# Kernel tuning notes

Hardware: AMD Instinct MI355X
Metric: run time of the kernel (lower is better)

## Reference

```python
import jax, jax.numpy as jnp
import numpy as np

B, S, D, H = 4, 2048, 768, 12
DK = D // H


def setup_inputs() -> dict:
    key = jax.random.key(0)
    ks = jax.random.split(key, 12)
    s = 1.0 / np.sqrt(D)
    return {
        "query": jax.random.normal(ks[0], (B, S, D), jnp.float32),
        "key_": jax.random.normal(ks[1], (B, S, D), jnp.float32),
        "value": jax.random.normal(ks[2], (B, S, D), jnp.float32),
        "mask": jax.random.randint(ks[3], (B, S), 0, 2, jnp.int32),
        # nn.Linear weights are (out_features, in_features); y = x @ W.T + b
        "Wq": jax.random.normal(ks[4], (D, D), jnp.float32) * s,
        "bq": jnp.zeros((D,), jnp.float32),
        "Wk": jax.random.normal(ks[5], (D, D), jnp.float32) * s,
        "bk": jnp.zeros((D,), jnp.float32),
        "Wv": jax.random.normal(ks[6], (D, D), jnp.float32) * s,
        "bv": jnp.zeros((D,), jnp.float32),
        "Wo": jax.random.normal(ks[7], (D, D), jnp.float32) * s,
        "bo": jnp.zeros((D,), jnp.float32),
    }


def reference(query, key_, value, mask, Wq, bq, Wk, bk, Wv, bv, Wo, bo):
    b = query.shape[0]
    # QKV projections, split heads: (B, S, D) -> (B, H, S, DK)
    def proj(x, W, bia):
        y = x @ W.T + bia
        return y.reshape(b, -1, H, DK).transpose(0, 2, 1, 3)

    q = proj(query, Wq, bq)
    k = proj(key_, Wk, bk)
    v = proj(value, Wv, bv)

    # Scaled dot-product attention with full [B, H, S, S] score matrix
    scores = jnp.einsum("bhqd,bhkd->bhqk", q, k) / jnp.sqrt(jnp.float32(DK))
    # mask: (B, S) broadcast over heads and query positions; masked_fill(mask==0, -1e9)
    scores = jnp.where(mask[:, None, None, :] == 0, jnp.float32(-1e9), scores)
    attn = jax.nn.softmax(scores, axis=-1)
    x = jnp.einsum("bhqk,bhkd->bhqd", attn, v)  # (B, H, S, DK)

    # merge heads and output projection
    x = x.transpose(0, 2, 1, 3).reshape(b, -1, H * DK)
    return x @ Wo.T + bo
```

## Files before the change

### kernel.cpp

```cpp
#include <hip/hip_runtime.h>
#include <math.h>

#define B_  4
#define S_  2048
#define D_  768
#define H_  12
#define DK_ 64
#define M_  (B_ * S_)
#define NBH_ (B_ * H_)

typedef float f32x4 __attribute__((ext_vector_type(4)));
typedef float f32x16 __attribute__((ext_vector_type(16)));
typedef __bf16 bf16x8 __attribute__((ext_vector_type(8)));
typedef unsigned u32x4v __attribute__((ext_vector_type(4)));

static __device__ __forceinline__ unsigned short f2bf(float f) {
    unsigned u = __builtin_bit_cast(unsigned, f);
    u += 0x7fffu + ((u >> 16) & 1u);
    return (unsigned short)(u >> 16);
}

static __device__ __forceinline__ unsigned cvt_pk_bf16(float lo, float hi) {
    unsigned r;
    asm("v_cvt_pk_bf16_f32 %0, %1, %2" : "=v"(r) : "v"(lo), "v"(hi));
    return r;
}

static __device__ __forceinline__ void proj_body(
    const float* __restrict__ X, const float* __restrict__ W,
    const float* __restrict__ bias, void* __restrict__ outp, const int mode,
    const float oscale)
{
    __shared__ __align__(16) unsigned short As[2][128 * 32];
    __shared__ __align__(16) unsigned short Bs[2][128 * 32];

    const int t  = threadIdx.x;
    const int l  = t & 63;
    const int w  = t >> 6;
    const int lr = l & 15;
    const int lg = l >> 4;
    const int wm = w >> 1;
    const int wn = w & 1;
    const int m0 = blockIdx.x * 128;
    const int n0 = blockIdx.y * 128;

    const int v0r = t >> 2,         v0s = t & 3;
    const int v1r = (t + 256) >> 2, v1s = (t + 256) & 3;
    const int off0 = v0r * 32 + ((v0s ^ ((v0r >> 1) & 3)) << 3);
    const int off1 = v1r * 32 + ((v1s ^ ((v1r >> 1) & 3)) << 3);
    const float* xg0 = X + (size_t)(m0 + v0r) * D_ + v0s * 8;
    const float* xg1 = X + (size_t)(m0 + v1r) * D_ + v1s * 8;
    const float* wg0 = W + (size_t)(n0 + v0r) * D_ + v0s * 8;
    const float* wg1 = W + (size_t)(n0 + v1r) * D_ + v1s * 8;

    float4 pxa, pxb, pxc, pxd, pwa, pwb, pwc, pwd;

#define PROJ_LOAD(K0) do { \
        pxa = *(const float4*)(xg0 + (K0)); pxb = *(const float4*)(xg0 + (K0) + 4); \
        pxc = *(const float4*)(xg1 + (K0)); pxd = *(const float4*)(xg1 + (K0) + 4); \
        pwa = *(const float4*)(wg0 + (K0)); pwb = *(const float4*)(wg0 + (K0) + 4); \
        pwc = *(const float4*)(wg1 + (K0)); pwd = *(const float4*)(wg1 + (K0) + 4); \
    } while (0)

#define PROJ_STORE(BUF) do { \
        u32x4v xa_, xb_, wa_, wb_; \
        xa_.x = cvt_pk_bf16(pxa.x, pxa.y); xa_.y = cvt_pk_bf16(pxa.z, pxa.w); \
        xa_.z = cvt_pk_bf16(pxb.x, pxb.y); xa_.w = cvt_pk_bf16(pxb.z, pxb.w); \
        xb_.x = cvt_pk_bf16(pxc.x, pxc.y); xb_.y = cvt_pk_bf16(pxc.z, pxc.w); \
        xb_.z = cvt_pk_bf16(pxd.x, pxd.y); xb_.w = cvt_pk_bf16(pxd.z, pxd.w); \
        wa_.x = cvt_pk_bf16(pwa.x, pwa.y); wa_.y = cvt_pk_bf16(pwa.z, pwa.w); \
        wa_.z = cvt_pk_bf16(pwb.x, pwb.y); wa_.w = cvt_pk_bf16(pwb.z, pwb.w); \
        wb_.x = cvt_pk_bf16(pwc.x, pwc.y); wb_.y = cvt_pk_bf16(pwc.z, pwc.w); \
        wb_.z = cvt_pk_bf16(pwd.x, pwd.y); wb_.w = cvt_pk_bf16(pwd.z, pwd.w); \
        *(u32x4v*)&As[BUF][off0] = xa_; \
        *(u32x4v*)&As[BUF][off1] = xb_; \
        *(u32x4v*)&Bs[BUF][off0] = wa_; \
        *(u32x4v*)&Bs[BUF][off1] = wb_; \
    } while (0)

    f32x4 acc[4][4];
#pragma unroll
    for (int mi = 0; mi < 4; mi++)
#pragma unroll
        for (int ni = 0; ni < 4; ni++) acc[mi][ni] = (f32x4){0.f, 0.f, 0.f, 0.f};

    const int fsw = (lr >> 1) & 3;

    PROJ_LOAD(0);
    PROJ_STORE(0);
    __syncthreads();

    for (int kt = 0; kt < 24; kt++) {
        const int cur = kt & 1;
        const bool more = (kt < 23);

        if (more) PROJ_LOAD((kt + 1) * 32);

        bf16x8 af[4], bfr[4];
#pragma unroll
        for (int mi = 0; mi < 4; mi++) {
            int row = wm * 64 + mi * 16 + lr;
            af[mi] = *(const bf16x8*)&As[cur][row * 32 + ((lg ^ fsw) << 3)];
        }
#pragma unroll
        for (int ni = 0; ni < 4; ni++) {
            int row = wn * 64 + ni * 16 + lr;
            bfr[ni] = *(const bf16x8*)&Bs[cur][row * 32 + ((lg ^ fsw) << 3)];
        }
#pragma unroll
        for (int mi = 0; mi < 4; mi++)
#pragma unroll
            for (int ni = 0; ni < 4; ni++)
                acc[mi][ni] = __builtin_amdgcn_mfma_f32_16x16x32_bf16(
                    af[mi], bfr[ni], acc[mi][ni], 0, 0, 0);

        if (more) PROJ_STORE(cur ^ 1);
        __syncthreads();
    }

#undef PROJ_LOAD
#undef PROJ_STORE

    const int mrow0 = m0 + wm * 64;
    const int ncol0 = n0 + wn * 64;
    if (mode == 1) {
        float* out = (float*)outp;
#pragma unroll
        for (int mi = 0; mi < 4; mi++)
#pragma unroll
            for (int ni = 0; ni < 4; ni++) {
                int n = ncol0 + ni * 16 + lr;
                float bv = bias[n];
#pragma unroll
                for (int j = 0; j < 4; j++) {
                    int m = mrow0 + mi * 16 + 4 * lg + j;
                    out[(size_t)m * D_ + n] = acc[mi][ni][j] + bv;
                }
            }
    } else if (mode == 0) {
        unsigned short* out = (unsigned short*)outp;
#pragma unroll
        for (int mi = 0; mi < 4; mi++)
#pragma unroll
            for (int ni = 0; ni < 4; ni++) {
                int n = ncol0 + ni * 16 + lr;
                int h = n >> 6, dk = n & 63;
                float bv = bias[n];
#pragma unroll
                for (int j = 0; j < 4; j++) {
                    int m = mrow0 + mi * 16 + 4 * lg + j;
                    int b = m >> 11, s = m & (S_ - 1);
                    out[((size_t)(b * H_ + h) * S_ + s) * DK_ + dk] =
                        f2bf((acc[mi][ni][j] + bv) * oscale);
                }
            }
    } else {
        unsigned short* out = (unsigned short*)outp;
#pragma unroll
        for (int mi = 0; mi < 4; mi++)
#pragma unroll
            for (int ni = 0; ni < 4; ni++) {
                int n = ncol0 + ni * 16 + lr;
                int h = n >> 6, dk = n & 63;
                float bv = bias[n];
                int m = mrow0 + mi * 16 + 4 * lg;
                int b = m >> 11, s = m & (S_ - 1);
                uint2 o;
                o.x = cvt_pk_bf16(acc[mi][ni][0] + bv, acc[mi][ni][1] + bv);
                o.y = cvt_pk_bf16(acc[mi][ni][2] + bv, acc[mi][ni][3] + bv);
                *(uint2*)&out[((size_t)(b * H_ + h) * DK_ + dk) * S_ + s] = o;
            }
    }
}

__global__ __launch_bounds__(256) void proj_qkv(
    const float* __restrict__ Xq, const float* __restrict__ Xk,
    const float* __restrict__ Xv,
    const float* __restrict__ Wq, const float* __restrict__ bq,
    const float* __restrict__ Wk, const float* __restrict__ bk,
    const float* __restrict__ Wv, const float* __restrict__ bv,
    unsigned short* __restrict__ Qb, unsigned short* __restrict__ Kb,
    unsigned short* __restrict__ VT)
{
    const int z = blockIdx.z;
    const float* X    = (z == 0) ? Xq : (z == 1) ? Xk : Xv;
    const float* W    = (z == 0) ? Wq : (z == 1) ? Wk : Wv;
    const float* bias = (z == 0) ? bq : (z == 1) ? bk : bv;
    void* out         = (z == 0) ? (void*)Qb : (z == 1) ? (void*)Kb : (void*)VT;
    const int mode    = (z == 2) ? 2 : 0;
    const float osc   = (z == 0) ? 0.125f : 1.0f;
    proj_body(X, W, bias, out, mode, osc);
}

__global__ __launch_bounds__(256) void proj_mfma(
    const float* __restrict__ X, const float* __restrict__ W,
    const float* __restrict__ bias, void* __restrict__ outp, const int mode,
    const float oscale)
{
    proj_body(X, W, bias, outp, mode, oscale);
}

__global__ __launch_bounds__(256) void attn_mfma(
    const unsigned short* __restrict__ Qb, const unsigned short* __restrict__ Kb,
    const unsigned short* __restrict__ VTb, const int* __restrict__ mask,
    float* __restrict__ O)
{
    __shared__ __align__(16) unsigned short Ks[2][64 * 64];
    __shared__ __align__(16) unsigned short Vs[2][64 * 64];

    const int tid = threadIdx.x;
    const int w  = tid >> 6;
    const int l  = tid & 63;
    const int q  = l & 31;
    const int hl = l >> 5;

    const int bh = blockIdx.x % NBH_;
    const int qt = blockIdx.x / NBH_;
    const int b  = bh / H_;
    const int hh = bh - b * H_;
    const int q0 = qt * 128 + w * 32;

    const unsigned short* qp = Qb + ((size_t)bh * S_ + q0 + q) * DK_;
    bf16x8 qf[4];
#pragma unroll
    for (int c = 0; c < 4; c++)
        qf[c] = *(const bf16x8*)(qp + c * 16 + hl * 8);

    const unsigned qext_sel = (hl == 0) ? 0x00003F80u : 0u;
    const unsigned bias_sel = (hl == 0) ? 0x0000C480u : 0u;
    u32x4v qe; qe.x = qext_sel; qe.y = 0u; qe.z = 0u; qe.w = 0u;
    const bf16x8 qf_ext = __builtin_bit_cast(bf16x8, qe);
    u32x4v on; on.x = on.y = on.z = on.w = 0x3F803F80u;
    const bf16x8 vOnes = __builtin_bit_cast(bf16x8, on);

    f32x16 acc0, acc1, accl;
#pragma unroll
    for (int i = 0; i < 16; i++) { acc0[i] = 0.f; acc1[i] = 0.f; accl[i] = 0.f; }

    const unsigned short* kbase = Kb + (size_t)bh * S_ * DK_;
    const unsigned short* vbase = VTb + (size_t)bh * DK_ * S_;
    const int* mbase = mask + b * S_;

    const int row0 = tid >> 3,         slot0 = tid & 7;
    const int row1 = (tid + 256) >> 3, slot1 = (tid + 256) & 7;
    const int ld0 = row0 * 64 + ((slot0 * 8) ^ ((row0 & 7) << 3));
    const int ld1 = row1 * 64 + ((slot1 * 8) ^ ((row1 & 7) << 3));
    const unsigned short* kg0 = kbase + row0 * DK_ + slot0 * 8;
    const unsigned short* kg1 = kbase + row1 * DK_ + slot1 * 8;
    const unsigned short* vg0 = vbase + (size_t)row0 * S_ + slot0 * 8;
    const unsigned short* vg1 = vbase + (size_t)row1 * S_ + slot1 * 8;

    {
        int4 kr0 = *(const int4*)(kg0);
        int4 kr1 = *(const int4*)(kg1);
        int4 vr0 = *(const int4*)(vg0);
        int4 vr1 = *(const int4*)(vg1);
        *(int4*)&Ks[0][ld0] = kr0;
        *(int4*)&Ks[0][ld1] = kr1;
        *(int4*)&Vs[0][ld0] = vr0;
        *(int4*)&Vs[0][ld1] = vr1;
    }
    __syncthreads();

    const int fsw = (q & 7) << 3;

    for (int tt = 0; tt < 32; tt++) {
        const int j0  = tt * 64;
        const int cur = tt & 1;
        const bool more = (tt < 31);

        int4 kr0, kr1, vr0, vr1;
        if (more) {
            kr0 = *(const int4*)(kg0 + (size_t)(j0 + 64) * DK_);
            kr1 = *(const int4*)(kg1 + (size_t)(j0 + 64) * DK_);
            vr0 = *(const int4*)(vg0 + (j0 + 64));
            vr1 = *(const int4*)(vg1 + (j0 + 64));
        }

        int mv0 = mbase[j0 + q];
        int mv1 = mbase[j0 + 32 + q];
        u32x4v bw0; bw0.x = (mv0 == 0) ? bias_sel : 0u; bw0.y = 0u; bw0.z = 0u; bw0.w = 0u;
        u32x4v bw1; bw1.x = (mv1 == 0) ? bias_sel : 0u; bw1.y = 0u; bw1.z = 0u; bw1.w = 0u;
        bf16x8 kExt0 = __builtin_bit_cast(bf16x8, bw0);
        bf16x8 kExt1 = __builtin_bit_cast(bf16x8, bw1);

        bf16x8 kA[2][4];
#pragma unroll
        for (int kf = 0; kf < 2; kf++)
#pragma unroll
            for (int c = 0; c < 4; c++)
                kA[kf][c] = *(const bf16x8*)&Ks[cur][(32 * kf + q) * 64 +
                                ((c * 16 + hl * 8) ^ fsw)];

        f32x16 s0, s1;
#pragma unroll
        for (int i = 0; i < 16; i++) { s0[i] = 0.f; s1[i] = 0.f; }
        __builtin_amdgcn_s_setprio(1);
#pragma unroll
        for (int c = 0; c < 4; c++) {
            s0 = __builtin_amdgcn_mfma_f32_32x32x16_bf16(kA[0][c], qf[c], s0, 0, 0, 0);
            s1 = __builtin_amdgcn_mfma_f32_32x32x16_bf16(kA[1][c], qf[c], s1, 0, 0, 0);
        }
        s0 = __builtin_amdgcn_mfma_f32_32x32x16_bf16(kExt0, qf_ext, s0, 0, 0, 0);
        s1 = __builtin_amdgcn_mfma_f32_32x32x16_bf16(kExt1, qf_ext, s1, 0, 0, 0);
        __builtin_amdgcn_s_setprio(0);

        bf16x8 vA[2][4];
#pragma unroll
        for (int db = 0; db < 2; db++)
#pragma unroll
            for (int c = 0; c < 4; c++)
                vA[db][c] = *(const bf16x8*)&Vs[cur][(32 * db + q) * 64 +
                                ((c * 16 + hl * 8) ^ fsw)];

        float pv[2][16];
#pragma unroll
        for (int r = 0; r < 16; r++) pv[0][r] = __expf(s0[r]);
#pragma unroll
        for (int r = 0; r < 16; r++) pv[1][r] = __expf(s1[r]);

        bf16x8 pb[4];
#pragma unroll
        for (int cp = 0; cp < 4; cp++) {
            const int kfi = cp >> 1;
            const int e0  = 8 * (cp & 1);
            unsigned lo0 = cvt_pk_bf16(pv[kfi][e0 + 0], pv[kfi][e0 + 1]);
            unsigned hi0 = cvt_pk_bf16(pv[kfi][e0 + 2], pv[kfi][e0 + 3]);
            unsigned lo1 = cvt_pk_bf16(pv[kfi][e0 + 4], pv[kfi][e0 + 5]);
            unsigned hi1 = cvt_pk_bf16(pv[kfi][e0 + 6], pv[kfi][e0 + 7]);
            asm("v_permlane32_swap_b32 %0, %1" : "+v"(lo0), "+v"(lo1));
            asm("v_permlane32_swap_b32 %0, %1" : "+v"(hi0), "+v"(hi1));
            u32x4v pw;
            pw.x = lo0; pw.y = hi0; pw.z = lo1; pw.w = hi1;
            pb[cp] = __builtin_bit_cast(bf16x8, pw);
        }

        __builtin_amdgcn_s_setprio(1);
#pragma unroll
        for (int cp = 0; cp < 4; cp++) {
            acc0 = __builtin_amdgcn_mfma_f32_32x32x16_bf16(vA[0][cp], pb[cp], acc0, 0, 0, 0);
            acc1 = __builtin_amdgcn_mfma_f32_32x32x16_bf16(vA[1][cp], pb[cp], acc1, 0, 0, 0);
            accl = __builtin_amdgcn_mfma_f32_32x32x16_bf16(vOnes,    pb[cp], accl, 0, 0, 0);
        }
        __builtin_amdgcn_s_setprio(0);

        if (more) {
            *(int4*)&Ks[cur ^ 1][ld0] = kr0;
            *(int4*)&Ks[cur ^ 1][ld1] = kr1;
            *(int4*)&Vs[cur ^ 1][ld0] = vr0;
            *(int4*)&Vs[cur ^ 1][ld1] = vr1;
        }
        __syncthreads();
    }

    float inv = 1.f / accl[0];
    float* ob = O + ((size_t)b * S_ + q0 + q) * D_ + hh * DK_;
#pragma unroll
    for (int b2 = 0; b2 < 4; b2++) {
        float4 o;
        o.x = acc0[4 * b2 + 0] * inv;
        o.y = acc0[4 * b2 + 1] * inv;
        o.z = acc0[4 * b2 + 2] * inv;
        o.w = acc0[4 * b2 + 3] * inv;
        *(float4*)(ob + 8 * b2 + 4 * hl) = o;
    }
#pragma unroll
    for (int b2 = 0; b2 < 4; b2++) {
        float4 o;
        o.x = acc1[4 * b2 + 0] * inv;
        o.y = acc1[4 * b2 + 1] * inv;
        o.z = acc1[4 * b2 + 2] * inv;
        o.w = acc1[4 * b2 + 3] * inv;
        *(float4*)(ob + 32 + 8 * b2 + 4 * hl) = o;
    }
}

extern "C" void kernel_launch(void* const* d_in, const int* in_sizes, int n_in,
                              void* d_out, int out_size, void* d_ws, size_t ws_size,
                              hipStream_t stream) {
    (void)in_sizes; (void)n_in; (void)out_size; (void)ws_size;

    const float* query = (const float*)d_in[0];
    const float* key_  = (const float*)d_in[1];
    const float* value = (const float*)d_in[2];
    const int*   mask  = (const int*)d_in[3];
    const float* Wq = (const float*)d_in[4];  const float* bq = (const float*)d_in[5];
    const float* Wk = (const float*)d_in[6];  const float* bk = (const float*)d_in[7];
    const float* Wv = (const float*)d_in[8];  const float* bv = (const float*)d_in[9];
    const float* Wo = (const float*)d_in[10]; const float* bo = (const float*)d_in[11];
    float* out = (float*)d_out;

    unsigned short* Qb = (unsigned short*)d_ws;
    unsigned short* Kb = Qb + (size_t)M_ * D_;
    unsigned short* VT = Kb + (size_t)M_ * D_;
    float*          Xb = (float*)(VT + (size_t)M_ * D_);

    dim3 gqkv(M_ / 128, D_ / 128, 3);
    proj_qkv<<<gqkv, 256, 0, stream>>>(query, key_, value,
                                       Wq, bq, Wk, bk, Wv, bv, Qb, Kb, VT);

    attn_mfma<<<dim3((S_ / 128) * NBH_), 256, 0, stream>>>(Qb, Kb, VT, mask, Xb);

    dim3 gproj(M_ / 128, D_ / 128);
    proj_mfma<<<gproj, 256, 0, stream>>>(Xb, Wo, bo, (void*)out, 1, 1.0f);
}
```

Measured before the change: 184.9 us.

## Stage K/V tiles via direct global-to-LDS loads with pre-swizzled global layout

The K and V^T projection epilogues now write their outputs in a pre-swizzled order, so the attention kernel can use global_load_lds (direct global-to-shared DMA) without applying the bank-conflict XOR at store time. This removes the register round trip and the explicit LDS stores in the attention kernel's double-buffered K/V pipeline, which should free VGPRs and issue slots. The cost is that the producer and consumer layouts are now coupled. Correctness depends on the waitcnt and barrier ordering around the async LDS writes.

```diff
diff --git a/kernel.cpp b/kernel.cpp
--- a/kernel.cpp
+++ b/kernel.cpp
@@ -24,6 +24,12 @@
     unsigned r;
     asm("v_cvt_pk_bf16_f32 %0, %1, %2" : "=v"(r) : "v"(lo), "v"(hi));
     return r;
+}
+
+static __device__ __forceinline__ void gload_lds16(const void* g, void* l) {
+    __builtin_amdgcn_global_load_lds(
+        (const __attribute__((address_space(1))) void*)g,
+        (__attribute__((address_space(3))) void*)l, 16, 0, 0);
 }
 
 static __device__ __forceinline__ void proj_body(
@@ -137,24 +143,7 @@
                     out[(size_t)m * D_ + n] = acc[mi][ni][j] + bv;
                 }
             }
-    } else if (mode == 0) {
-        unsigned short* out = (unsigned short*)outp;
-#pragma unroll
-        for (int mi = 0; mi < 4; mi++)
-#pragma unroll
-            for (int ni = 0; ni < 4; ni++) {
-                int n = ncol0 + ni * 16 + lr;
-                int h = n >> 6, dk = n & 63;
-                float bv = bias[n];
-#pragma unroll
-                for (int j = 0; j < 4; j++) {
-                    int m = mrow0 + mi * 16 + 4 * lg + j;
-                    int b = m >> 11, s = m & (S_ - 1);
-                    out[((size_t)(b * H_ + h) * S_ + s) * DK_ + dk] =
-                        f2bf((acc[mi][ni][j] + bv) * oscale);
-                }
-            }
-    } else {
+    } else if (mode == 2) {
         unsigned short* out = (unsigned short*)outp;
 #pragma unroll
         for (int mi = 0; mi < 4; mi++)
@@ -165,10 +154,31 @@
                 float bv = bias[n];
                 int m = mrow0 + mi * 16 + 4 * lg;
                 int b = m >> 11, s = m & (S_ - 1);
+                int slotp = ((s >> 3) & 7) ^ (dk & 7);
+                int ssw = (s & ~63) | (slotp << 3) | (s & 7);
                 uint2 o;
                 o.x = cvt_pk_bf16(acc[mi][ni][0] + bv, acc[mi][ni][1] + bv);
                 o.y = cvt_pk_bf16(acc[mi][ni][2] + bv, acc[mi][ni][3] + bv);
-                *(uint2*)&out[((size_t)(b * H_ + h) * DK_ + dk) * S_ + s] = o;
+                *(uint2*)&out[((size_t)(b * H_ + h) * DK_ + dk) * S_ + ssw] = o;
+            }
+    } else {
+        unsigned short* out = (unsigned short*)outp;
+#pragma unroll
+        for (int mi = 0; mi < 4; mi++)
+#pragma unroll
+            for (int ni = 0; ni < 4; ni++) {
+                int n = ncol0 + ni * 16 + lr;
+                int h = n >> 6, dk = n & 63;
+                float bv = bias[n];
+#pragma unroll
+                for (int j = 0; j < 4; j++) {
+                    int m = mrow0 + mi * 16 + 4 * lg + j;
+                    int b = m >> 11, s = m & (S_ - 1);
+                    int dko = (mode == 3)
+                        ? ((dk & 7) | ((((dk >> 3) ^ (s & 7))) << 3)) : dk;
+                    out[((size_t)(b * H_ + h) * S_ + s) * DK_ + dko] =
+                        f2bf((acc[mi][ni][j] + bv) * oscale);
+                }
             }
     }
 }
@@ -187,7 +197,7 @@
     const float* W    = (z == 0) ? Wq : (z == 1) ? Wk : Wv;
     const float* bias = (z == 0) ? bq : (z == 1) ? bk : bv;
     void* out         = (z == 0) ? (void*)Qb : (z == 1) ? (void*)Kb : (void*)VT;
-    const int mode    = (z == 2) ? 2 : 0;
+    const int mode    = (z == 0) ? 0 : (z == 1) ? 3 : 2;
     const float osc   = (z == 0) ? 0.125f : 1.0f;
     proj_body(X, W, bias, out, mode, osc);
 }
@@ -241,25 +251,18 @@
     const unsigned short* vbase = VTb + (size_t)bh * DK_ * S_;
     const int* mbase = mask + b * S_;
 
-    const int row0 = tid >> 3,         slot0 = tid & 7;
-    const int row1 = (tid + 256) >> 3, slot1 = (tid + 256) & 7;
-    const int ld0 = row0 * 64 + ((slot0 * 8) ^ ((row0 & 7) << 3));
-    const int ld1 = row1 * 64 + ((slot1 * 8) ^ ((row1 & 7) << 3));
-    const unsigned short* kg0 = kbase + row0 * DK_ + slot0 * 8;
-    const unsigned short* kg1 = kbase + row1 * DK_ + slot1 * 8;
-    const unsigned short* vg0 = vbase + (size_t)row0 * S_ + slot0 * 8;
-    const unsigned short* vg1 = vbase + (size_t)row1 * S_ + slot1 * 8;
-
-    {
-        int4 kr0 = *(const int4*)(kg0);
-        int4 kr1 = *(const int4*)(kg1);
-        int4 vr0 = *(const int4*)(vg0);
-        int4 vr1 = *(const int4*)(vg1);
-        *(int4*)&Ks[0][ld0] = kr0;
-        *(int4*)&Ks[0][ld1] = kr1;
-        *(int4*)&Vs[0][ld0] = vr0;
-        *(int4*)&Vs[0][ld1] = vr1;
-    }
+    const unsigned short* kdma = kbase + (16 * w) * DK_ + l * 8;
+    const unsigned short* vdma0 = vbase + (size_t)(16 * w + (l >> 3)) * S_ + (l & 7) * 8;
+    const unsigned short* vdma1 = vdma0 + (size_t)8 * S_;
+
+#define STAGE_DMA(J0, NB) do { \
+        gload_lds16(kdma + (size_t)(J0) * DK_,            &Ks[NB][(16 * w) * 64]); \
+        gload_lds16(kdma + (size_t)(J0) * DK_ + 8 * DK_,  &Ks[NB][(16 * w + 8) * 64]); \
+        gload_lds16(vdma0 + (J0),                         &Vs[NB][(16 * w) * 64]); \
+        gload_lds16(vdma1 + (J0),                         &Vs[NB][(16 * w + 8) * 64]); \
+    } while (0)
+
+    STAGE_DMA(0, 0);
     __syncthreads();
 
     const int fsw = (q & 7) << 3;
@@ -267,14 +270,9 @@
     for (int tt = 0; tt < 32; tt++) {
         const int j0  = tt * 64;
         const int cur = tt & 1;
-        const bool more = (tt < 31);
-
-        int4 kr0, kr1, vr0, vr1;
-        if (more) {
-            kr0 = *(const int4*)(kg0 + (size_t)(j0 + 64) * DK_);
-            kr1 = *(const int4*)(kg1 + (size_t)(j0 + 64) * DK_);
-            vr0 = *(const int4*)(vg0 + (j0 + 64));
-            vr1 = *(const int4*)(vg1 + (j0 + 64));
+
+        if (tt < 31) {
+            if (cur) STAGE_DMA(j0 + 64, 0); else STAGE_DMA(j0 + 64, 1);
         }
 
         int mv0 = mbase[j0 + q];
@@ -344,14 +342,9 @@
         }
         __builtin_amdgcn_s_setprio(0);
 
-        if (more) {
-            *(int4*)&Ks[cur ^ 1][ld0] = kr0;
-            *(int4*)&Ks[cur ^ 1][ld1] = kr1;
-            *(int4*)&Vs[cur ^ 1][ld0] = vr0;
-            *(int4*)&Vs[cur ^ 1][ld1] = vr1;
-        }
         __syncthreads();
     }
+#undef STAGE_DMA
 
     float inv = 1.f / accl[0];
     float* ob = O + ((size_t)b * S_ + q0 + q) * D_ + hh * DK_;
```

After: 189.8 us. 2.7% more time.
